# Kernel tuning notes

Hardware: AMD Instinct MI355X
Metric: run time of the kernel (lower is better)

Reference implementation:

```python
import jax, jax.numpy as jnp
import numpy as np

TEMPERATURE = 0.1  # InfoNCE default
K_POS, K_NEG = 5, 10


def _l2norm(x, eps):
    return x / jnp.maximum(jnp.linalg.norm(x, axis=-1, keepdims=True), eps)


def setup_inputs() -> dict:
    key = jax.random.key(0)
    k1, k2 = jax.random.split(key)
    anchor = jax.random.normal(k1, (4096, 512), dtype=jnp.float32)
    sample = jax.random.normal(k2, (4096, 512), dtype=jnp.float32)
    return {"anchor": anchor, "sample": sample}


def reference(anchor, sample):
    N = anchor.shape[0]
    # Pairwise cosine similarity (torch.cosine_similarity eps=1e-8), computed
    a = _l2norm(anchor, 1e-8)
    sim = a @ a.T  # (N, N)

    # topk largest=True (5 nearest) and largest=False (10 farthest)
    _, pos_idx = jax.lax.top_k(sim, K_POS)    # (N, 5)
    _, neg_idx = jax.lax.top_k(-sim, K_NEG)   # (N, 10), ascending sim

    # Faithful replication of the original gather/repeat pattern:
    # query = sample.repeat(5, 1) -> tiling (index i maps to sample[i % N])
    query = jnp.tile(sample, (K_POS, 1))                          # (5N, d)
    pos = sample[pos_idx.reshape(-1)]                             # (5N, d) anchor-major
    neg = sample[neg_idx.reshape(-1)].reshape(N, K_NEG, -1)       # (N, 10, d)
    neg = jnp.repeat(neg, K_POS, axis=0)                          # (5N, 10, d)

    # InfoNCE (negative_mode='paired'): F.normalize (eps=1e-12) then logits.
    q = _l2norm(query, 1e-12)
    p = _l2norm(pos, 1e-12)
    n = _l2norm(neg, 1e-12)
    pos_logit = jnp.sum(q * p, axis=1, keepdims=True)             # (5N, 1)
    neg_logits = jnp.einsum('bd,bkd->bk', q, n)                   # (5N, 10)
    logits = jnp.concatenate([pos_logit, neg_logits], axis=1) / TEMPERATURE
    # cross_entropy with labels == 0, mean reduction
    loss = -jnp.mean(jax.nn.log_softmax(logits, axis=1)[:, 0])
    return loss
```

## Files before the change

### kernel.cpp

```cpp
#include <hip/hip_runtime.h>
#include <math.h>

#define N 4096
#define D 512
#define KPOS 5
#define KNEG 10
#define NB 32
#define NPAIR (NB * (NB - 1) / 2)
#define NJOB (2 * NPAIR + 2 * NB)

typedef short s16x8 __attribute__((ext_vector_type(8)));
typedef unsigned short u16x8 __attribute__((ext_vector_type(8)));
typedef unsigned u32x4 __attribute__((ext_vector_type(4)));
typedef float f32x4 __attribute__((ext_vector_type(4)));

__device__ __forceinline__ unsigned short f2bf(float x) {
    unsigned u = __float_as_uint(x);
    unsigned r = (u + 0x7FFFu + ((u >> 16) & 1u)) >> 16;
    return (unsigned short)r;
}
__device__ __forceinline__ unsigned short mapbf(float x) {
    const unsigned short h = f2bf(x);
    return h ^ ((h & 0x8000u) ? 0xFFFFu : 0x8000u);
}
__device__ __forceinline__ unsigned umax_(unsigned a, unsigned b) { return a > b ? a : b; }
__device__ __forceinline__ unsigned umin_(unsigned a, unsigned b) { return a < b ? a : b; }
__device__ __forceinline__ unsigned pkmax(unsigned a, unsigned b) {
    unsigned r; asm("v_pk_max_u16 %0, %1, %2" : "=v"(r) : "v"(a), "v"(b)); return r;
}
__device__ __forceinline__ unsigned pkmin(unsigned a, unsigned b) {
    unsigned r; asm("v_pk_min_u16 %0, %1, %2" : "=v"(r) : "v"(a), "v"(b)); return r;
}

#define DPPU(old, v, ctrl, rm) \
    ((unsigned)__builtin_amdgcn_update_dpp((int)(old), (int)(v), (ctrl), (rm), 0xF, false))

__device__ __forceinline__ unsigned wave_max_b(unsigned v) {
    v = umax_(v, DPPU(0u, v, 0x121, 0xF));
    v = umax_(v, DPPU(0u, v, 0x122, 0xF));
    v = umax_(v, DPPU(0u, v, 0x124, 0xF));
    v = umax_(v, DPPU(0u, v, 0x128, 0xF));
    v = umax_(v, DPPU(0u, v, 0x142, 0xA));
    v = umax_(v, DPPU(0u, v, 0x143, 0xC));
    return (unsigned)__builtin_amdgcn_readlane((int)v, 63);
}
__device__ __forceinline__ unsigned wave_min_b(unsigned v) {
    v = umin_(v, DPPU(0xFFFFFFFFu, v, 0x121, 0xF));
    v = umin_(v, DPPU(0xFFFFFFFFu, v, 0x122, 0xF));
    v = umin_(v, DPPU(0xFFFFFFFFu, v, 0x124, 0xF));
    v = umin_(v, DPPU(0xFFFFFFFFu, v, 0x128, 0xF));
    v = umin_(v, DPPU(0xFFFFFFFFu, v, 0x142, 0xA));
    v = umin_(v, DPPU(0xFFFFFFFFu, v, 0x143, 0xC));
    return (unsigned)__builtin_amdgcn_readlane((int)v, 63);
}
__device__ __forceinline__ float row_allmax_f(float v) {
    v = fmaxf(v, __uint_as_float(DPPU(0xFF800000u, __float_as_uint(v), 0x121, 0xF)));
    v = fmaxf(v, __uint_as_float(DPPU(0xFF800000u, __float_as_uint(v), 0x122, 0xF)));
    v = fmaxf(v, __uint_as_float(DPPU(0xFF800000u, __float_as_uint(v), 0x124, 0xF)));
    v = fmaxf(v, __uint_as_float(DPPU(0xFF800000u, __float_as_uint(v), 0x128, 0xF)));
    return v;
}
__device__ __forceinline__ float row_allsum_f(float v) {
    v += __uint_as_float(DPPU(0u, __float_as_uint(v), 0x121, 0xF));
    v += __uint_as_float(DPPU(0u, __float_as_uint(v), 0x122, 0xF));
    v += __uint_as_float(DPPU(0u, __float_as_uint(v), 0x124, 0xF));
    v += __uint_as_float(DPPU(0u, __float_as_uint(v), 0x128, 0xF));
    return v;
}
__device__ __forceinline__ float wave_sum_f(float v) {
    v = row_allsum_f(v);
    v += __uint_as_float(DPPU(0u, __float_as_uint(v), 0x142, 0xA));
    v += __uint_as_float(DPPU(0u, __float_as_uint(v), 0x143, 0xC));
    return __uint_as_float((unsigned)__builtin_amdgcn_readlane((int)__float_as_uint(v), 63));
}

__global__ __launch_bounds__(256) void norm_kernel(const float* __restrict__ anchor,
                                                   const float* __restrict__ sample,
                                                   unsigned short* __restrict__ Abf,
                                                   unsigned short* __restrict__ s_norm) {
    const int wave = threadIdx.x >> 6, lane = threadIdx.x & 63;
    const int row = blockIdx.x * 4 + wave;
    const bool is_anchor = row < N;
    const float* in = is_anchor ? anchor + (size_t)row * D
                                : sample + (size_t)(row - N) * D;
    const float eps = is_anchor ? 1e-8f : 1e-12f;

    const float4 v0 = *(const float4*)&in[lane * 4];
    const float4 v1 = *(const float4*)&in[256 + lane * 4];
    float ss = v0.x * v0.x + v0.y * v0.y + v0.z * v0.z + v0.w * v0.w
             + v1.x * v1.x + v1.y * v1.y + v1.z * v1.z + v1.w * v1.w;
#pragma unroll
    for (int off = 32; off > 0; off >>= 1) ss += __shfl_xor(ss, off);
    const float inv = 1.0f / fmaxf(sqrtf(ss), eps);

    unsigned short* out = is_anchor ? Abf + (size_t)row * D
                                    : s_norm + (size_t)(row - N) * D;
    ushort4 o0, o1;
    o0.x = f2bf(v0.x * inv); o0.y = f2bf(v0.y * inv);
    o0.z = f2bf(v0.z * inv); o0.w = f2bf(v0.w * inv);
    o1.x = f2bf(v1.x * inv); o1.y = f2bf(v1.y * inv);
    o1.z = f2bf(v1.z * inv); o1.w = f2bf(v1.w * inv);
    *(ushort4*)&out[lane * 4] = o0;
    *(ushort4*)&out[256 + lane * 4] = o1;
}

#define ATILE (128 * 64)
#define BTILE (64 * 64)

__device__ __forceinline__ void stage_ab(const unsigned short* __restrict__ A,
                                         unsigned short* As, unsigned short* Bs,
                                         int rowA, int colB, int kl, int t) {
#pragma unroll
    for (int i = 0; i < 4; ++i) {
        const int c = i * 256 + t;
        const int r = c >> 3;
        const int ke = ((c & 7) ^ (r & 7)) * 8;
        __builtin_amdgcn_global_load_lds(
            (const __attribute__((address_space(1))) void*)(A + (size_t)(rowA + r) * D + kl + ke),
            (__attribute__((address_space(3))) void*)(As + c * 8), 16, 0, 0);
    }
#pragma unroll
    for (int i = 0; i < 2; ++i) {
        const int c = i * 256 + t;
        const int r = c >> 3;
        const int ke = ((c & 7) ^ (r & 7)) * 8;
        __builtin_amdgcn_global_load_lds(
            (const __attribute__((address_space(1))) void*)(A + (size_t)(colB + r) * D + kl + ke),
            (__attribute__((address_space(3))) void*)(Bs + c * 8), 16, 0, 0);
    }
}

__global__ __launch_bounds__(256) void gemm_bf16(const unsigned short* __restrict__ Abf,
                                                 unsigned short* __restrict__ C) {
    const int q = (blockIdx.x % 8) * (NJOB / 8) + blockIdx.x / 8;

    int bi, bj, h;
    if (q < 2 * NPAIR) {
        const int op = q >> 1;
        h = q & 1;
        bi = (int)(31.5f - sqrtf(31.5f * 31.5f - 2.f * (float)op));
        while (31 * bi - bi * (bi - 1) / 2 > op) --bi;
        while (31 * (bi + 1) - (bi + 1) * bi / 2 <= op) ++bi;
        bj = bi + 1 + (op - (31 * bi - bi * (bi - 1) / 2));
    } else {
        const int d = q - 2 * NPAIR;
        bi = bj = d >> 1;
        h = d & 1;
    }

    __shared__ __align__(16) unsigned short As[2 * ATILE];
    __shared__ __align__(16) unsigned short Bs[2 * BTILE];

    const int t = threadIdx.x;
    const int l = t & 63;
    const int w = t >> 6;
    const int wr = w >> 1, wc = w & 1;
    const int rowA = bi * 128;
    const int colB = bj * 128 + h * 64;
    const int lrow = l & 15, lgrp = l >> 4;

    f32x4 acc[4][2];
#pragma unroll
    for (int m = 0; m < 4; ++m)
#pragma unroll
        for (int n = 0; n < 2; ++n) acc[m][n] = (f32x4){0.f, 0.f, 0.f, 0.f};

    stage_ab(Abf, As, Bs, rowA, colB, 0, t);
    __syncthreads();

    for (int kc = 0; kc < 8; ++kc) {
        const int cur = kc & 1;
        if (kc < 7)
            stage_ab(Abf, As + (cur ^ 1) * ATILE, Bs + (cur ^ 1) * BTILE,
                     rowA, colB, (kc + 1) * 64, t);

        const char* AsB = (const char*)(As + cur * ATILE);
        const char* BsB = (const char*)(Bs + cur * BTILE);
#pragma unroll
        for (int kk = 0; kk < 2; ++kk) {
            s16x8 af[4], bfr[2];
#pragma unroll
            for (int m = 0; m < 4; ++m) {
                const int row = wr * 64 + m * 16 + lrow;
                af[m] = *(const s16x8*)(AsB + row * 128 + (((kk * 4 + lgrp) ^ (row & 7)) * 16));
            }
#pragma unroll
            for (int n = 0; n < 2; ++n) {
                const int row = wc * 32 + n * 16 + lrow;
                bfr[n] = *(const s16x8*)(BsB + row * 128 + (((kk * 4 + lgrp) ^ (row & 7)) * 16));
            }
#pragma unroll
            for (int m = 0; m < 4; ++m)
#pragma unroll
                for (int n = 0; n < 2; ++n)
                    acc[m][n] = __builtin_amdgcn_mfma_f32_16x16x32_bf16(af[m], bfr[n], acc[m][n], 0, 0, 0);
        }
        __syncthreads();
    }

    unsigned short* Tn = As;
    unsigned short* Tm = Bs;
#pragma unroll
    for (int m = 0; m < 4; ++m) {
#pragma unroll
        for (int n = 0; n < 2; ++n) {
            const int c = wc * 32 + n * 16 + lrow;
            const int r0 = wr * 64 + m * 16 + lgrp * 4;
#pragma unroll
            for (int j = 0; j < 4; ++j) {
                const unsigned short val = mapbf(acc[m][n][j]);
                Tn[(r0 + j) * 64 + c] = val;
                Tm[c * 128 + ((r0 + j) ^ ((c & 7) << 3))] = val;
            }
        }
    }
    __syncthreads();

#pragma unroll
    for (int i = 0; i < 4; ++i) {
        const int chunk = i * 256 + t;
        const int r = chunk >> 3;
        const int c8 = (chunk & 7) * 8;
        const u16x8 v = *(const u16x8*)&Tn[r * 64 + c8];
        __builtin_nontemporal_store(v, (u16x8*)&C[(size_t)(rowA + r) * N + colB + c8]);
    }
    if (bi != bj) {
#pragma unroll
        for (int i = 0; i < 4; ++i) {
            const int chunk = i * 256 + t;
            const int c = chunk >> 4;
            const int r8 = (chunk & 15) * 8;
            const u16x8 v = *(const u16x8*)&Tm[c * 128 + (r8 ^ ((c & 7) << 3))];
            __builtin_nontemporal_store(v, (u16x8*)&C[(size_t)(colB + c) * N + rowA + r8]);
        }
    }
}

__device__ __forceinline__ void ins_top(unsigned* tk, unsigned c) {
#pragma unroll
    for (int q = 0; q < KPOS - 1; ++q) {
        const unsigned x = umax_(tk[q], c);
        c = umin_(tk[q], c);
        tk[q] = x;
    }
    tk[KPOS - 1] = umax_(tk[KPOS - 1], c);
}
__device__ __forceinline__ void ins_bot(unsigned* bk, unsigned c) {
#pragma unroll
    for (int q = 0; q < KNEG - 1; ++q) {
        const unsigned x = umin_(bk[q], c);
        c = umax_(bk[q], c);
        bk[q] = x;
    }
    bk[KNEG - 1] = umin_(bk[KNEG - 1], c);
}

__global__ __launch_bounds__(256) void fused_topk_loss(const unsigned short* __restrict__ sim,
                                                       const unsigned short* __restrict__ s_norm,
                                                       float* __restrict__ partials) {
    __shared__ float wsum[4];
    __shared__ unsigned cand_top[4][256];
    __shared__ unsigned cand_bot[4][256];
    __shared__ unsigned cnt[4][2];
    const int wave = threadIdx.x >> 6, lane = threadIdx.x & 63;
    const int ia = blockIdx.x * 4 + wave;
    const unsigned short* s = sim + (size_t)ia * N;
    const int cc = lane & 15;
    const int g = lane >> 4;

    if (lane == 0) { cnt[wave][0] = 0u; cnt[wave][1] = 0u; }

    const u32x4 d0 = __builtin_bit_cast(u32x4, __builtin_nontemporal_load((const u16x8*)&s[8 * lane]));
    const u32x4 d1 = __builtin_bit_cast(u32x4, __builtin_nontemporal_load((const u16x8*)&s[8 * (lane + 64)]));
    const u32x4 d2 = __builtin_bit_cast(u32x4, __builtin_nontemporal_load((const u16x8*)&s[8 * (lane + 128)]));
    const u32x4 d3 = __builtin_bit_cast(u32x4, __builtin_nontemporal_load((const u16x8*)&s[8 * (lane + 192)]));
    const u32x4 d4 = __builtin_bit_cast(u32x4, __builtin_nontemporal_load((const u16x8*)&s[8 * (lane + 256)]));
    const u32x4 d5 = __builtin_bit_cast(u32x4, __builtin_nontemporal_load((const u16x8*)&s[8 * (lane + 320)]));
    const u32x4 d6 = __builtin_bit_cast(u32x4, __builtin_nontemporal_load((const u16x8*)&s[8 * (lane + 384)]));
    const u32x4 d7 = __builtin_bit_cast(u32x4, __builtin_nontemporal_load((const u16x8*)&s[8 * (lane + 448)]));
    __builtin_amdgcn_sched_barrier(0);
    asm volatile("" ::: "memory");

#define VMAX(v) pkmax(pkmax(v.x, v.y), pkmax(v.z, v.w))
#define VMIN(v) pkmin(pkmin(v.x, v.y), pkmin(v.z, v.w))
    unsigned mx = VMAX(d0), mn = VMIN(d0);
    mx = pkmax(mx, VMAX(d1)); mn = pkmin(mn, VMIN(d1));
    mx = pkmax(mx, VMAX(d2)); mn = pkmin(mn, VMIN(d2));
    mx = pkmax(mx, VMAX(d3)); mn = pkmin(mn, VMIN(d3));
    mx = pkmax(mx, VMAX(d4)); mn = pkmin(mn, VMIN(d4));
    mx = pkmax(mx, VMAX(d5)); mn = pkmin(mn, VMIN(d5));
    mx = pkmax(mx, VMAX(d6)); mn = pkmin(mn, VMIN(d6));
    mx = pkmax(mx, VMAX(d7)); mn = pkmin(mn, VMIN(d7));
#undef VMAX
#undef VMIN
    const unsigned lm = umax_(mx >> 16, mx & 0xFFFFu);
    const unsigned ln = umin_(mn >> 16, mn & 0xFFFFu);

    unsigned lo = 0u, hi = 0xFFFFu;
    while (lo < hi) {
        const unsigned mid = (lo + hi + 1u) >> 1;
        const int c = __popcll(__ballot(lm >= mid));
        if (c >= KPOS) lo = mid; else hi = mid - 1u;
    }
    const unsigned T5 = lo;
    lo = 0u; hi = 0xFFFFu;
    while (lo < hi) {
        const unsigned mid = (lo + hi) >> 1;
        const int c = __popcll(__ballot(ln <= mid));
        if (c >= KNEG) hi = mid; else lo = mid + 1u;
    }
    const unsigned T10 = lo;

    const unsigned t5g = (T5 == 0u) ? 0u : T5 - 1u;
    const unsigned t10g = (T10 >= 0xFFFFu) ? 0xFFFFu : T10 + 1u;
    const unsigned pair5 = t5g * 0x10001u;
    const unsigned pairA = t10g * 0x10001u;

#define SCAN_DW(dd, base)                                                      \
    {                                                                          \
        const unsigned pt = pkmax(dd, pair5);                                  \
        const unsigned pb = pkmin(dd, pairA);                                  \
        if (pt != pair5 || pb != pairA) {                                      \
            const unsigned ee0 = (dd) & 0xFFFFu, ee1 = (dd) >> 16;             \
            if (ee0 >= T5) { unsigned p = atomicAdd(&cnt[wave][0], 1u);        \
                cand_top[wave][p & 255u] = (ee0 << 16) | (unsigned)((base) ^ 0xFFF); } \
            if (ee1 >= T5) { unsigned p = atomicAdd(&cnt[wave][0], 1u);        \
                cand_top[wave][p & 255u] = (ee1 << 16) | (unsigned)(((base) + 1) ^ 0xFFF); } \
            if (ee0 <= T10) { unsigned p = atomicAdd(&cnt[wave][1], 1u);       \
                cand_bot[wave][p & 255u] = (ee0 << 16) | (unsigned)(base); }   \
            if (ee1 <= T10) { unsigned p = atomicAdd(&cnt[wave][1], 1u);       \
                cand_bot[wave][p & 255u] = (ee1 << 16) | (unsigned)((base) + 1); } \
        }                                                                      \
    }
#define SCAN_VEC(dv, vb)                                                       \
    SCAN_DW(dv.x, (vb));      SCAN_DW(dv.y, (vb) + 2);                         \
    SCAN_DW(dv.z, (vb) + 4);  SCAN_DW(dv.w, (vb) + 6);
    SCAN_VEC(d0, 8 * lane)
    SCAN_VEC(d1, 8 * (lane + 64))
    SCAN_VEC(d2, 8 * (lane + 128))
    SCAN_VEC(d3, 8 * (lane + 192))
    SCAN_VEC(d4, 8 * (lane + 256))
    SCAN_VEC(d5, 8 * (lane + 320))
    SCAN_VEC(d6, 8 * (lane + 384))
    SCAN_VEC(d7, 8 * (lane + 448))
#undef SCAN_VEC
#undef SCAN_DW

    const unsigned ctT = umin_(cnt[wave][0], 256u);
    const unsigned ctB = umin_(cnt[wave][1], 256u);
    unsigned tk[KPOS], bk[KNEG];
#pragma unroll
    for (int q = 0; q < KPOS; ++q) tk[q] = 0u;
#pragma unroll
    for (int q = 0; q < KNEG; ++q) bk[q] = 0xFFFFFFFFu;
    for (unsigned c = lane; c < ctT; c += 64) ins_top(tk, cand_top[wave][c]);
    for (unsigned c = lane; c < ctB; c += 64) ins_bot(bk, cand_bot[wave][c]);

    int rowB = 0;
#pragma unroll
    for (int it = 0; it < KPOS; ++it) {
        const unsigned m = wave_max_b(tk[0]);
        if (cc == it) rowB = (int)((m & 0xFFFu) ^ 0xFFFu);
        if (tk[0] == m) {
#pragma unroll
            for (int q = 0; q < KPOS - 1; ++q) tk[q] = tk[q + 1];
            tk[KPOS - 1] = 0u;
        }
    }
#pragma unroll
    for (int it = 0; it < KNEG; ++it) {
        const unsigned m = wave_min_b(bk[0]);
        if (cc == KPOS + it) rowB = (int)(m & 0xFFFu);
        if (bk[0] == m) {
#pragma unroll
            for (int q = 0; q < KNEG - 1; ++q) bk[q] = bk[q + 1];
            bk[KNEG - 1] = 0xFFFFFFFFu;
        }
    }

    const int rowA = (ia * KPOS + ((cc < KPOS) ? cc : 0)) & (N - 1);
    const unsigned short* pA = s_norm + (size_t)rowA * D + g * 8;
    const unsigned short* pB = s_norm + (size_t)rowB * D + g * 8;

    s16x8 a[16], b[16];
#pragma unroll
    for (int kk = 0; kk < 16; ++kk) {
        a[kk] = *(const s16x8*)(pA + kk * 32);
        b[kk] = *(const s16x8*)(pB + kk * 32);
    }
    __builtin_amdgcn_sched_barrier(0);
    asm volatile("" ::: "memory");

    f32x4 acc = (f32x4){0.f, 0.f, 0.f, 0.f};
#pragma unroll
    for (int kk = 0; kk < 16; ++kk)
        acc = __builtin_amdgcn_mfma_f32_16x16x32_bf16(a[kk], b[kk], acc, 0, 0, 0);

    float lsum = 0.f;
#pragma unroll
    for (int j = 0; j < 4; ++j) {
        const int p = g * 4 + j;
        const float logit = acc[j] * 10.f;
        const bool isneg = (cc >= KPOS) && (cc < 15);
        const bool ispos = (cc == p);
        const float x = (ispos || isneg) ? logit : -__builtin_inff();
        const float m = row_allmax_f(x);
        const float e = (ispos || isneg) ? expf(logit - m) : 0.f;
        const float sx = row_allsum_f(e);
        const float l0 = row_allsum_f(ispos ? logit : 0.f);
        if (p < KPOS && ispos) lsum += logf(sx) + m - l0;
    }

    const float ltot = wave_sum_f(lsum);
    if (lane == 0) wsum[wave] = ltot;
    __syncthreads();
    if (threadIdx.x == 0)
        partials[blockIdx.x] = wsum[0] + wsum[1] + wsum[2] + wsum[3];
}

__global__ __launch_bounds__(256) void reduce_kernel(const float* __restrict__ partials,
                                                     float* __restrict__ out) {
    __shared__ float wsum[4];
    const int wave = threadIdx.x >> 6, lane = threadIdx.x & 63;
    float s = partials[threadIdx.x] + partials[threadIdx.x + 256] +
              partials[threadIdx.x + 512] + partials[threadIdx.x + 768];
#pragma unroll
    for (int off = 32; off > 0; off >>= 1) s += __shfl_xor(s, off);
    if (lane == 0) wsum[wave] = s;
    __syncthreads();
    if (threadIdx.x == 0)
        *out = (wsum[0] + wsum[1] + wsum[2] + wsum[3]) * (1.0f / (float)(N * KPOS));
}

extern "C" void kernel_launch(void* const* d_in, const int* in_sizes, int n_in,
                              void* d_out, int out_size, void* d_ws, size_t ws_size,
                              hipStream_t stream) {
    const float* anchor = (const float*)d_in[0];
    const float* sample = (const float*)d_in[1];
    float* out = (float*)d_out;

    char* ws = (char*)d_ws;
    unsigned short* Abf    = (unsigned short*)ws;
    unsigned short* s_norm = (unsigned short*)(ws + (size_t)4 * 1024 * 1024);
    unsigned short* sim    = (unsigned short*)(ws + (size_t)8 * 1024 * 1024);
    float* partials = (float*)(ws + (size_t)40 * 1024 * 1024);

    norm_kernel<<<2048, 256, 0, stream>>>(anchor, sample, Abf, s_norm);

    gemm_bf16<<<NJOB, 256, 0, stream>>>(Abf, sim);

    fused_topk_loss<<<N / 4, 256, 0, stream>>>(sim, s_norm, partials);

    reduce_kernel<<<1, 256, 0, stream>>>(partials, out);
}
```

Baseline: 60.15 us.

## Split each similarity row across two waves and merge top-k through shared memory

Each anchor row of the similarity matrix is now scanned by two waves, each covering half the columns, instead of one wave covering all of them. Each wave computes its local top-5 and bottom-10 and writes them to shared memory. After a block barrier, the first wave of each pair merges its partner's candidates and runs the MFMA loss computation. The grid doubles and the per-thread register load halves, which aims to raise occupancy and memory-level parallelism. The cost is an extra merge step, a block-wide sync, and half the waves sitting idle during the loss phase.

```diff
diff --git a/kernel.cpp b/kernel.cpp
--- a/kernel.cpp
+++ b/kernel.cpp
@@ -258,26 +258,26 @@
 __global__ __launch_bounds__(256) void fused_topk_loss(const unsigned short* __restrict__ sim,
                                                        const unsigned short* __restrict__ s_norm,
                                                        float* __restrict__ partials) {
-    __shared__ float wsum[4];
+    __shared__ float wsum[2];
     __shared__ unsigned cand_top[4][256];
     __shared__ unsigned cand_bot[4][256];
     __shared__ unsigned cnt[4][2];
+    __shared__ unsigned ltop[4][KPOS];
+    __shared__ unsigned lbot[4][KNEG];
     const int wave = threadIdx.x >> 6, lane = threadIdx.x & 63;
-    const int ia = blockIdx.x * 4 + wave;
+    const int ia = blockIdx.x * 2 + (wave >> 1);
+    const int half = wave & 1;
     const unsigned short* s = sim + (size_t)ia * N;
+    const int hb = half * 2048;
     const int cc = lane & 15;
     const int g = lane >> 4;
 
     if (lane == 0) { cnt[wave][0] = 0u; cnt[wave][1] = 0u; }
 
-    const u32x4 d0 = __builtin_bit_cast(u32x4, __builtin_nontemporal_load((const u16x8*)&s[8 * lane]));
-    const u32x4 d1 = __builtin_bit_cast(u32x4, __builtin_nontemporal_load((const u16x8*)&s[8 * (lane + 64)]));
-    const u32x4 d2 = __builtin_bit_cast(u32x4, __builtin_nontemporal_load((const u16x8*)&s[8 * (lane + 128)]));
-    const u32x4 d3 = __builtin_bit_cast(u32x4, __builtin_nontemporal_load((const u16x8*)&s[8 * (lane + 192)]));
-    const u32x4 d4 = __builtin_bit_cast(u32x4, __builtin_nontemporal_load((const u16x8*)&s[8 * (lane + 256)]));
-    const u32x4 d5 = __builtin_bit_cast(u32x4, __builtin_nontemporal_load((const u16x8*)&s[8 * (lane + 320)]));
-    const u32x4 d6 = __builtin_bit_cast(u32x4, __builtin_nontemporal_load((const u16x8*)&s[8 * (lane + 384)]));
-    const u32x4 d7 = __builtin_bit_cast(u32x4, __builtin_nontemporal_load((const u16x8*)&s[8 * (lane + 448)]));
+    const u32x4 d0 = __builtin_bit_cast(u32x4, __builtin_nontemporal_load((const u16x8*)&s[hb + 8 * lane]));
+    const u32x4 d1 = __builtin_bit_cast(u32x4, __builtin_nontemporal_load((const u16x8*)&s[hb + 8 * (lane + 64)]));
+    const u32x4 d2 = __builtin_bit_cast(u32x4, __builtin_nontemporal_load((const u16x8*)&s[hb + 8 * (lane + 128)]));
+    const u32x4 d3 = __builtin_bit_cast(u32x4, __builtin_nontemporal_load((const u16x8*)&s[hb + 8 * (lane + 192)]));
     __builtin_amdgcn_sched_barrier(0);
     asm volatile("" ::: "memory");
 
@@ -287,10 +287,6 @@
     mx = pkmax(mx, VMAX(d1)); mn = pkmin(mn, VMIN(d1));
     mx = pkmax(mx, VMAX(d2)); mn = pkmin(mn, VMIN(d2));
     mx = pkmax(mx, VMAX(d3)); mn = pkmin(mn, VMIN(d3));
-    mx = pkmax(mx, VMAX(d4)); mn = pkmin(mn, VMIN(d4));
-    mx = pkmax(mx, VMAX(d5)); mn = pkmin(mn, VMIN(d5));
-    mx = pkmax(mx, VMAX(d6)); mn = pkmin(mn, VMIN(d6));
-    mx = pkmax(mx, VMAX(d7)); mn = pkmin(mn, VMIN(d7));
 #undef VMAX
 #undef VMIN
     const unsigned lm = umax_(mx >> 16, mx & 0xFFFFu);
@@ -335,14 +331,10 @@
 #define SCAN_VEC(dv, vb)                                                       \
     SCAN_DW(dv.x, (vb));      SCAN_DW(dv.y, (vb) + 2);                         \
     SCAN_DW(dv.z, (vb) + 4);  SCAN_DW(dv.w, (vb) + 6);
-    SCAN_VEC(d0, 8 * lane)
-    SCAN_VEC(d1, 8 * (lane + 64))
-    SCAN_VEC(d2, 8 * (lane + 128))
-    SCAN_VEC(d3, 8 * (lane + 192))
-    SCAN_VEC(d4, 8 * (lane + 256))
-    SCAN_VEC(d5, 8 * (lane + 320))
-    SCAN_VEC(d6, 8 * (lane + 384))
-    SCAN_VEC(d7, 8 * (lane + 448))
+    SCAN_VEC(d0, hb + 8 * lane)
+    SCAN_VEC(d1, hb + 8 * (lane + 64))
+    SCAN_VEC(d2, hb + 8 * (lane + 128))
+    SCAN_VEC(d3, hb + 8 * (lane + 192))
 #undef SCAN_VEC
 #undef SCAN_DW
 
@@ -356,11 +348,11 @@
     for (unsigned c = lane; c < ctT; c += 64) ins_top(tk, cand_top[wave][c]);
     for (unsigned c = lane; c < ctB; c += 64) ins_bot(bk, cand_bot[wave][c]);
 
-    int rowB = 0;
+    unsigned wt[KPOS], wb[KNEG];
 #pragma unroll
     for (int it = 0; it < KPOS; ++it) {
         const unsigned m = wave_max_b(tk[0]);
-        if (cc == it) rowB = (int)((m & 0xFFFu) ^ 0xFFFu);
+        wt[it] = m;
         if (tk[0] == m) {
 #pragma unroll
             for (int q = 0; q < KPOS - 1; ++q) tk[q] = tk[q + 1];
@@ -370,7 +362,7 @@
 #pragma unroll
     for (int it = 0; it < KNEG; ++it) {
         const unsigned m = wave_min_b(bk[0]);
-        if (cc == KPOS + it) rowB = (int)(m & 0xFFFu);
+        wb[it] = m;
         if (bk[0] == m) {
 #pragma unroll
             for (int q = 0; q < KNEG - 1; ++q) bk[q] = bk[q + 1];
@@ -378,52 +370,76 @@
         }
     }
 
-    const int rowA = (ia * KPOS + ((cc < KPOS) ? cc : 0)) & (N - 1);
-    const unsigned short* pA = s_norm + (size_t)rowA * D + g * 8;
-    const unsigned short* pB = s_norm + (size_t)rowB * D + g * 8;
-
-    s16x8 a[16], b[16];
-#pragma unroll
-    for (int kk = 0; kk < 16; ++kk) {
-        a[kk] = *(const s16x8*)(pA + kk * 32);
-        b[kk] = *(const s16x8*)(pB + kk * 32);
-    }
-    __builtin_amdgcn_sched_barrier(0);
-    asm volatile("" ::: "memory");
-
-    f32x4 acc = (f32x4){0.f, 0.f, 0.f, 0.f};
-#pragma unroll
-    for (int kk = 0; kk < 16; ++kk)
-        acc = __builtin_amdgcn_mfma_f32_16x16x32_bf16(a[kk], b[kk], acc, 0, 0, 0);
-
-    float lsum = 0.f;
-#pragma unroll
-    for (int j = 0; j < 4; ++j) {
-        const int p = g * 4 + j;
-        const float logit = acc[j] * 10.f;
-        const bool isneg = (cc >= KPOS) && (cc < 15);
-        const bool ispos = (cc == p);
-        const float x = (ispos || isneg) ? logit : -__builtin_inff();
-        const float m = row_allmax_f(x);
-        const float e = (ispos || isneg) ? expf(logit - m) : 0.f;
-        const float sx = row_allsum_f(e);
-        const float l0 = row_allsum_f(ispos ? logit : 0.f);
-        if (p < KPOS && ispos) lsum += logf(sx) + m - l0;
-    }
-
-    const float ltot = wave_sum_f(lsum);
-    if (lane == 0) wsum[wave] = ltot;
+    if (lane == 0) {
+#pragma unroll
+        for (int i = 0; i < KPOS; ++i) ltop[wave][i] = wt[i];
+#pragma unroll
+        for (int i = 0; i < KNEG; ++i) lbot[wave][i] = wb[i];
+    }
+    __syncthreads();
+
+    if (half == 0) {
+#pragma unroll
+        for (int i = 0; i < KPOS; ++i) ins_top(wt, ltop[wave + 1][i]);
+#pragma unroll
+        for (int i = 0; i < KNEG; ++i) ins_bot(wb, lbot[wave + 1][i]);
+
+        int rowB = 0;
+#pragma unroll
+        for (int it = 0; it < KPOS; ++it)
+            if (cc == it) rowB = (int)((wt[it] & 0xFFFu) ^ 0xFFFu);
+#pragma unroll
+        for (int it = 0; it < KNEG; ++it)
+            if (cc == KPOS + it) rowB = (int)(wb[it] & 0xFFFu);
+
+        const int rowA = (ia * KPOS + ((cc < KPOS) ? cc : 0)) & (N - 1);
+        const unsigned short* pA = s_norm + (size_t)rowA * D + g * 8;
+        const unsigned short* pB = s_norm + (size_t)rowB * D + g * 8;
+
+        s16x8 a[16], b[16];
+#pragma unroll
+        for (int kk = 0; kk < 16; ++kk) {
+            a[kk] = *(const s16x8*)(pA + kk * 32);
+            b[kk] = *(const s16x8*)(pB + kk * 32);
+        }
+        __builtin_amdgcn_sched_barrier(0);
+        asm volatile("" ::: "memory");
+
+        f32x4 acc = (f32x4){0.f, 0.f, 0.f, 0.f};
+#pragma unroll
+        for (int kk = 0; kk < 16; ++kk)
+            acc = __builtin_amdgcn_mfma_f32_16x16x32_bf16(a[kk], b[kk], acc, 0, 0, 0);
+
+        float lsum = 0.f;
+#pragma unroll
+        for (int j = 0; j < 4; ++j) {
+            const int p = g * 4 + j;
+            const float logit = acc[j] * 10.f;
+            const bool isneg = (cc >= KPOS) && (cc < 15);
+            const bool ispos = (cc == p);
+            const float x = (ispos || isneg) ? logit : -__builtin_inff();
+            const float m = row_allmax_f(x);
+            const float e = (ispos || isneg) ? expf(logit - m) : 0.f;
+            const float sx = row_allsum_f(e);
+            const float l0 = row_allsum_f(ispos ? logit : 0.f);
+            if (p < KPOS && ispos) lsum += logf(sx) + m - l0;
+        }
+
+        const float ltot = wave_sum_f(lsum);
+        if (lane == 0) wsum[wave >> 1] = ltot;
+    }
     __syncthreads();
     if (threadIdx.x == 0)
-        partials[blockIdx.x] = wsum[0] + wsum[1] + wsum[2] + wsum[3];
+        partials[blockIdx.x] = wsum[0] + wsum[1];
 }
 
 __global__ __launch_bounds__(256) void reduce_kernel(const float* __restrict__ partials,
                                                      float* __restrict__ out) {
     __shared__ float wsum[4];
     const int wave = threadIdx.x >> 6, lane = threadIdx.x & 63;
-    float s = partials[threadIdx.x] + partials[threadIdx.x + 256] +
-              partials[threadIdx.x + 512] + partials[threadIdx.x + 768];
+    float s = 0.f;
+#pragma unroll
+    for (int i = 0; i < 8; ++i) s += partials[threadIdx.x + 256 * i];
 #pragma unroll
     for (int off = 32; off > 0; off >>= 1) s += __shfl_xor(s, off);
     if (lane == 0) wsum[wave] = s;
@@ -449,7 +465,7 @@
 
     gemm_bf16<<<NJOB, 256, 0, stream>>>(Abf, sim);
 
-    fused_topk_loss<<<N / 4, 256, 0, stream>>>(sim, s_norm, partials);
+    fused_topk_loss<<<N / 2, 256, 0, stream>>>(sim, s_norm, partials);
 
     reduce_kernel<<<1, 256, 0, stream>>>(partials, out);
 }
```

After: 65.95 us. 9.7% more time.
